# Performance work log

Hardware: AMD Instinct MI355X
Metric: run time of the kernel (lower is better)

Reference implementation:

```python
import jax, jax.numpy as jnp
import numpy as np

B, T, D = 2, 2048, 1024
H = 16
DH = D // H
SCALE = DH ** -0.5


def setup_inputs() -> dict:
    key = jax.random.key(0)
    ks = jax.random.split(key, 9)
    s = D ** -0.5
    return {
        "x": jax.random.normal(ks[0], (B, T, D), dtype=jnp.float32),
        "Wq": jax.random.normal(ks[1], (D, D), dtype=jnp.float32) * s,
        "bq": jax.random.normal(ks[2], (D,), dtype=jnp.float32) * 0.01,
        "Wk": jax.random.normal(ks[3], (D, D), dtype=jnp.float32) * s,
        "bk": jax.random.normal(ks[4], (D,), dtype=jnp.float32) * 0.01,
        "Wv": jax.random.normal(ks[5], (D, D), dtype=jnp.float32) * s,
        "bv": jax.random.normal(ks[6], (D,), dtype=jnp.float32) * 0.01,
        "Wo": jax.random.normal(ks[7], (D, D), dtype=jnp.float32) * s,
        "bo": jax.random.normal(ks[8], (D,), dtype=jnp.float32) * 0.01,
    }


def reference(x, Wq, bq, Wk, bk, Wv, bv, Wo, bo):
    # projections; torch Linear: y = x @ W.T + b. Here W is stored as (in, out).
    q = (x @ Wq + bq).reshape(B, T, H, DH).transpose(0, 2, 1, 3)  # (B,H,T,DH)
    k = (x @ Wk + bk).reshape(B, T, H, DH).transpose(0, 2, 1, 3)
    v = (x @ Wv + bv).reshape(B, T, H, DH).transpose(0, 2, 1, 3)
    scores = jnp.einsum("bhqd,bhkd->bhqk", q, k) * SCALE  # (B,H,T,T)
    causal = jnp.tril(jnp.ones((T, T), dtype=bool))
    scores = jnp.where(causal, scores, -jnp.inf)
    probs = jax.nn.softmax(scores, axis=-1)
    out = jnp.einsum("bhqk,bhkd->bhqd", probs, v)  # (B,H,T,DH)
    out = out.transpose(0, 2, 1, 3).reshape(B, T, D)
    out = out @ Wo + bo
    return out, (k, v)
```

## Files before the change

kernel.cpp:

```cpp
#include <hip/hip_runtime.h>

typedef float  f32x4  __attribute__((ext_vector_type(4)));
typedef float  f32x16 __attribute__((ext_vector_type(16)));
typedef __bf16 bf16x8 __attribute__((ext_vector_type(8)));
typedef short  s16x8  __attribute__((ext_vector_type(8)));
typedef short  s16x4  __attribute__((ext_vector_type(4)));
typedef unsigned int u32x4 __attribute__((ext_vector_type(4)));

static __device__ __forceinline__ unsigned short f2bf(float f) {
  return __builtin_bit_cast(unsigned short, (__bf16)f);
}
static __device__ __forceinline__ bf16x8 bc8(s16x8 v) {
  return __builtin_bit_cast(bf16x8, v);
}
static __device__ __forceinline__ f32x16 mfma32(bf16x8 a, bf16x8 b, f32x16 c) {
  return __builtin_amdgcn_mfma_f32_32x32x16_bf16(a, b, c, 0, 0, 0);
}
static __device__ __forceinline__ f32x4 mfma16(bf16x8 a, bf16x8 b, f32x4 c) {
  return __builtin_amdgcn_mfma_f32_16x16x32_bf16(a, b, c, 0, 0, 0);
}

static __device__ __forceinline__ void gl2lds16(const unsigned short* g, unsigned short* l) {
  __builtin_amdgcn_global_load_lds(
      (const __attribute__((address_space(1))) unsigned int*)g,
      (__attribute__((address_space(3))) unsigned int*)l, 16, 0, 0);
}

#define GSYNC(NSTR)                                          \
  do {                                                       \
    __builtin_amdgcn_sched_barrier(0);                       \
    asm volatile("s_waitcnt vmcnt(" NSTR ")" ::: "memory");  \
    __builtin_amdgcn_s_barrier();                            \
    __builtin_amdgcn_sched_barrier(0);                       \
  } while (0)

__global__ void prep_k(const float* __restrict__ x, unsigned short* __restrict__ xb,
                       const float* __restrict__ W0, const float* __restrict__ W1,
                       const float* __restrict__ W2, const float* __restrict__ W3,
                       unsigned short* __restrict__ wtb) {
  __shared__ unsigned short tl[64][72];
  const int bid = blockIdx.x;
  const int t = threadIdx.x;
  if (bid < 2048) {
    int i = (bid * 256 + t) * 8;
    float4 a = *(const float4*)(x + i);
    float4 b = *(const float4*)(x + i + 4);
    s16x8 o;
    o[0] = (short)f2bf(a.x); o[1] = (short)f2bf(a.y);
    o[2] = (short)f2bf(a.z); o[3] = (short)f2bf(a.w);
    o[4] = (short)f2bf(b.x); o[5] = (short)f2bf(b.y);
    o[6] = (short)f2bf(b.z); o[7] = (short)f2bf(b.w);
    *(s16x8*)(xb + i) = o;
    return;
  }
  const int rid = bid - 2048;
  const int z = rid >> 8, rem = rid & 255;
  const float* W = z == 0 ? W0 : z == 1 ? W1 : z == 2 ? W2 : W3;
  unsigned short* out = wtb + (size_t)z * 1048576;
  const int nt = (rem & 15) * 64, kt = (rem >> 4) * 64;
  const int row = t >> 2, seg = t & 3;
  const float* src = W + (kt + row) * 1024 + nt + seg * 16;
#pragma unroll
  for (int q = 0; q < 4; ++q) {
    float4 v = *(const float4*)(src + q * 4);
    tl[seg * 16 + q * 4 + 0][row] = f2bf(v.x);
    tl[seg * 16 + q * 4 + 1][row] = f2bf(v.y);
    tl[seg * 16 + q * 4 + 2][row] = f2bf(v.z);
    tl[seg * 16 + q * 4 + 3][row] = f2bf(v.w);
  }
  __syncthreads();
  unsigned short* dst = out + (nt + row) * 1024 + kt + seg * 16;
  *(s16x8*)dst       = *(const s16x8*)&tl[row][seg * 16];
  *(s16x8*)(dst + 8) = *(const s16x8*)&tl[row][seg * 16 + 8];
}

static __device__ __forceinline__ int trans_ix(int m, int n) {
  int b = m >> 11, tt = m & 2047, h = n >> 6, dh = n & 63;
  return ((b << 4) + h) * 131072 + tt * 64 + dh;
}

__global__ __launch_bounds__(512, 4) void gemm_qkv_k(const unsigned short* __restrict__ A,
                                                     const unsigned short* __restrict__ BT,
                                                     const float* __restrict__ b0,
                                                     const float* __restrict__ b1,
                                                     const float* __restrict__ b2,
                                                     float* __restrict__ outF,
                                                     unsigned short* __restrict__ oq,
                                                     unsigned short* __restrict__ ok,
                                                     unsigned short* __restrict__ ovT) {
  extern __shared__ unsigned short lds[];
  const int t = threadIdx.x;
  const int lane = t & 63, ln = lane & 15, g = lane >> 4;
  const int w = t >> 6, wm = w >> 2, wn = w & 3;
  const unsigned wgid = blockIdx.x;
  const unsigned swz = (wgid & 7) * 64 + (wgid >> 3);
  const int by = swz & 31, bx = swz >> 5;
  const int bm0 = by * 128, bn0 = bx * 192;

  const int ar = t >> 2;
  const unsigned short* aBase = A + (size_t)(bm0 + ar) * 1024 + (((t & 3) ^ ((ar >> 1) & 3)) * 8);
  const int br = t >> 3;
  const int bcol = (t & 7) ^ (br & 7);
  const unsigned short* bBase = BT + (size_t)(bn0 + br) * 1024 + bcol * 8;

  auto issueA = [&](int buf, int H, int kt) {
    gl2lds16(aBase + kt + H * 32, &lds[buf * 20480 + H * 4096 + t * 8]);
  };
  auto issueB = [&](int buf, int j, int kt) {
    gl2lds16(bBase + (size_t)j * 65536 + kt, &lds[buf * 20480 + 8192 + j * 4096 + t * 8]);
  };
  auto ldA = [&](int buf, int H, int mf) -> bf16x8 {
    const int row = wm * 64 + mf * 16 + ln;
    const int sp = g ^ ((row >> 1) & 3);
    return bc8(*(const s16x8*)&lds[buf * 20480 + H * 4096 + row * 32 + sp * 8]);
  };
  auto ldB = [&](int buf, int H, int nf) -> bf16x8 {
    const int row = wn * 48 + nf * 16 + ln;
    const int sp = (H * 4 + g) ^ (row & 7);
    return bc8(*(const s16x8*)&lds[buf * 20480 + 8192 + row * 64 + sp * 8]);
  };

  f32x4 acc[4][3] = {};
  issueA(0, 0, 0);
  issueB(0, 0, 0);
  issueB(0, 1, 0);
  issueB(0, 2, 0);
  issueA(0, 1, 0);

  for (int ti = 0; ti < 16; ++ti) {
    const int buf = ti & 1, nb = buf ^ 1;
    const bool hn = ti < 15;
    const int kn = (ti + 1) * 64;

    GSYNC("1");
    if (hn) { issueA(nb, 0, kn); issueB(nb, 0, kn); issueB(nb, 1, kn); }
    {
      bf16x8 afr[4], bfr[3];
#pragma unroll
      for (int mf = 0; mf < 4; ++mf) afr[mf] = ldA(buf, 0, mf);
#pragma unroll
      for (int nf = 0; nf < 3; ++nf) bfr[nf] = ldB(buf, 0, nf);
      __builtin_amdgcn_s_setprio(1);
#pragma unroll
      for (int mf = 0; mf < 4; ++mf)
#pragma unroll
        for (int nf = 0; nf < 3; ++nf) acc[mf][nf] = mfma16(afr[mf], bfr[nf], acc[mf][nf]);
      __builtin_amdgcn_s_setprio(0);
    }
    if (hn) GSYNC("3"); else GSYNC("0");
    if (hn) { issueB(nb, 2, kn); issueA(nb, 1, kn); }
    {
      bf16x8 afr[4], bfr[3];
#pragma unroll
      for (int mf = 0; mf < 4; ++mf) afr[mf] = ldA(buf, 1, mf);
#pragma unroll
      for (int nf = 0; nf < 3; ++nf) bfr[nf] = ldB(buf, 1, nf);
      __builtin_amdgcn_s_setprio(1);
#pragma unroll
      for (int mf = 0; mf < 4; ++mf)
#pragma unroll
        for (int nf = 0; nf < 3; ++nf) acc[mf][nf] = mfma16(afr[mf], bfr[nf], acc[mf][nf]);
      __builtin_amdgcn_s_setprio(0);
    }
  }

#pragma unroll
  for (int nf = 0; nf < 3; ++nf) {
    const int n = bn0 + wn * 48 + nf * 16 + ln;
    const int n1 = n & 1023;
    const float* bp = n < 1024 ? b0 : (n < 2048 ? b1 : b2);
    const float bias = bp[n1];
    if (n < 1024) {
#pragma unroll
      for (int mf = 0; mf < 4; ++mf)
#pragma unroll
        for (int r = 0; r < 4; ++r) {
          const int m = bm0 + wm * 64 + mf * 16 + g * 4 + r;
          oq[trans_ix(m, n1)] = f2bf((acc[mf][nf][r] + bias) * 0.18033688f);
        }
    } else if (n < 2048) {
#pragma unroll
      for (int mf = 0; mf < 4; ++mf)
#pragma unroll
        for (int r = 0; r < 4; ++r) {
          const int m = bm0 + wm * 64 + mf * 16 + g * 4 + r;
          const float v = acc[mf][nf][r] + bias;
          const int ix = trans_ix(m, n1);
          ok[ix] = f2bf(v);
          outF[4194304 + ix] = v;
        }
    } else {
      const int dh = n1 & 63, hh = n1 >> 6;
#pragma unroll
      for (int mf = 0; mf < 4; ++mf) {
        const int m0 = bm0 + wm * 64 + mf * 16 + g * 4;
        const int bb = m0 >> 11, tt = m0 & 2047;
        s16x4 pv;
#pragma unroll
        for (int r = 0; r < 4; ++r) {
          const float v = acc[mf][nf][r] + bias;
          outF[8388608 + trans_ix(m0 + r, n1)] = v;
          pv[r] = (short)f2bf(v);
        }
        *(s16x4*)(ovT + (size_t)((bb << 4) + hh) * 131072 + (size_t)dh * 2048 + tt) = pv;
      }
    }
  }
}

__global__ __launch_bounds__(512, 4) void gemm_o_k(const unsigned short* __restrict__ A,
                                                   const unsigned short* __restrict__ BT,
                                                   const float* __restrict__ b0,
                                                   float* __restrict__ outF) {
  extern __shared__ unsigned short lds[];
  const int t = threadIdx.x;
  const int lane = t & 63, ln = lane & 15, g = lane >> 4;
  const int w = t >> 6, wm = w >> 2, wn = w & 3;
  const unsigned wgid = blockIdx.x;
  const unsigned swz = (wgid & 7) * 64 + (wgid >> 3);
  const int bx = swz & 7, by = swz >> 3;
  const int bm0 = by * 64, bn0 = bx * 128;

  const int row = t >> 3;
  const int scol = (t & 7) ^ (row & 7);
  const unsigned short* aSrc = A + (size_t)(bm0 + row) * 1024 + scol * 8;
  const unsigned short* bSrc0 = BT + (size_t)(bn0 + row) * 1024 + scol * 8;
  const unsigned short* bSrc1 = BT + (size_t)(bn0 + 64 + row) * 1024 + scol * 8;

  auto issue3 = [&](int buf, int ti) {
    const int kt = ti * 64;
    gl2lds16(aSrc + kt, &lds[buf * 12288 + t * 8]);
    gl2lds16(bSrc0 + kt, &lds[buf * 12288 + 4096 + t * 8]);
    gl2lds16(bSrc1 + kt, &lds[buf * 12288 + 8192 + t * 8]);
  };
  auto ldA = [&](int buf, int H, int mf) -> bf16x8 {
    const int r = wm * 32 + mf * 16 + ln;
    const int sp = (H * 4 + g) ^ (r & 7);
    return bc8(*(const s16x8*)&lds[buf * 12288 + r * 64 + sp * 8]);
  };
  auto ldB = [&](int buf, int H, int nf) -> bf16x8 {
    const int r = wn * 32 + nf * 16 + ln;
    const int j = r >> 6, rl = r & 63;
    const int sp = (H * 4 + g) ^ (rl & 7);
    return bc8(*(const s16x8*)&lds[buf * 12288 + 4096 + j * 4096 + rl * 64 + sp * 8]);
  };

  f32x4 acc[2][2] = {};
  issue3(0, 0);
  issue3(1, 1);

  for (int i = 0; i < 16; ++i) {
    const int buf = i & 1;
    if (i < 15) GSYNC("3"); else GSYNC("0");
    bf16x8 a0[2], a1[2], bq0[2], bq1[2];
#pragma unroll
    for (int mf = 0; mf < 2; ++mf) { a0[mf] = ldA(buf, 0, mf); a1[mf] = ldA(buf, 1, mf); }
#pragma unroll
    for (int nf = 0; nf < 2; ++nf) { bq0[nf] = ldB(buf, 0, nf); bq1[nf] = ldB(buf, 1, nf); }
    asm volatile("s_waitcnt lgkmcnt(0)" ::: "memory");
    __builtin_amdgcn_sched_barrier(0);
    __builtin_amdgcn_s_barrier();
    __builtin_amdgcn_sched_barrier(0);
    if (i + 2 < 16) issue3(buf, i + 2);
    __builtin_amdgcn_s_setprio(1);
#pragma unroll
    for (int mf = 0; mf < 2; ++mf)
#pragma unroll
      for (int nf = 0; nf < 2; ++nf) {
        acc[mf][nf] = mfma16(a0[mf], bq0[nf], acc[mf][nf]);
        acc[mf][nf] = mfma16(a1[mf], bq1[nf], acc[mf][nf]);
      }
    __builtin_amdgcn_s_setprio(0);
  }

#pragma unroll
  for (int nf = 0; nf < 2; ++nf) {
    const int n = bn0 + wn * 32 + nf * 16 + ln;
    const float bias = b0[n];
#pragma unroll
    for (int mf = 0; mf < 2; ++mf)
#pragma unroll
      for (int r = 0; r < 4; ++r) {
        const int m = bm0 + wm * 32 + mf * 16 + g * 4 + r;
        outF[(size_t)m * 1024 + n] = acc[mf][nf][r] + bias;
      }
  }
}

__global__ __launch_bounds__(512) void attn_k(const unsigned short* __restrict__ qb,
                                              const unsigned short* __restrict__ kb,
                                              const unsigned short* __restrict__ vbT,
                                              unsigned short* __restrict__ ob) {
  extern __shared__ s16x8 kvS[];
  const int t = threadIdx.x;
  const int lane = t & 63, l31 = lane & 31, h5 = lane >> 5;
  const int w = t >> 6, grp = w >> 2, qw = w & 3;
  const unsigned wg = blockIdx.x;
  const int x = wg & 7, r_ = wg >> 3;
  const int bh = x + 8 * (r_ >> 3);
  const int p = r_ & 7;
  const int b = bh >> 4, h = bh & 15;
  const unsigned short* Qp = qb + (size_t)bh * 131072;
  const unsigned short* Kp = kb + (size_t)bh * 131072;
  const unsigned short* Vp = vbT + (size_t)bh * 131072;

  const int e0 = qw * 64 + lane;
  const int kr0 = e0 >> 3;
  const int kcol = (e0 & 7) ^ (kr0 & 7);
  const unsigned short* kSrc = Kp + (size_t)kr0 * 64 + kcol * 8;
  const unsigned short* vSrc = Vp + (size_t)kr0 * 2048 + kcol * 8;
  s16x8* gB = &kvS[grp * 3072];

  s16x8 onesv;
#pragma unroll
  for (int z = 0; z < 8; ++z) onesv[z] = (short)0x3F80;
  const bf16x8 onesf = bc8(onesv);

  float* mg0 = (float*)&kvS[0];
  float* mg1 = mg0 + 4352;
  float* ml  = mg0 + 8704;
  const int slot = qw * 64 + lane;

  for (int half = 0; half < 2; ++half) {
    const int qblk = half == 0 ? p : 15 - p;
    const int q0 = qblk * 128;
    const int NT = qblk + 1;
    const int tbase = grp * NT;
    const int qg = q0 + qw * 32 + l31;

    __syncthreads();

    bf16x8 qf[4];
#pragma unroll
    for (int m = 0; m < 4; ++m)
      qf[m] = bc8(*(const s16x8*)(Qp + (size_t)qg * 64 + 16 * m + 8 * h5));

    auto issue = [&](int ti, int buf) {
      const int kv0 = (tbase + ti) * 64;
      unsigned short* kd = (unsigned short*)&gB[buf * 1024];
      unsigned short* vd = (unsigned short*)&gB[buf * 1024 + 512];
      const unsigned short* ks = kSrc + (size_t)kv0 * 64;
      const unsigned short* vs = vSrc + kv0;
      gl2lds16(ks,         kd + e0 * 8);
      gl2lds16(ks + 2048,  kd + (e0 + 256) * 8);
      gl2lds16(vs,         vd + e0 * 8);
      gl2lds16(vs + 65536, vd + (e0 + 256) * 8);
    };

    issue(0, 0);
    if (NT > 1) issue(1, 1);

    f32x16 o0 = {}, o1 = {}, lsum = {};
    int buf = 0;
    for (int i = 0; i < NT; ++i) {
      if (i + 1 < NT) GSYNC("4"); else GSYNC("0");
      if (i + 2 < NT) issue(i + 2, buf == 0 ? 2 : buf - 1);
      const int kv0 = (tbase + i) * 64;
      const bool active = (kv0 <= q0 + qw * 32 + 31);
      if (active) {
        const s16x8* kb_ = &gB[buf * 1024];
        const s16x8* vb2 = &gB[buf * 1024 + 512];
        f32x16 s0 = {}, s1 = {};
#pragma unroll
        for (int m = 0; m < 4; ++m) {
          const int sl = 2 * m + h5;
          bf16x8 a0 = bc8(kb_[l31 * 8 + (sl ^ (l31 & 7))]);
          bf16x8 a1 = bc8(kb_[(l31 + 32) * 8 + (sl ^ (l31 & 7))]);
          s0 = mfma32(a0, qf[m], s0);
          s1 = mfma32(a1, qf[m], s1);
        }
        if (kv0 + 63 > q0 + qw * 32) {
#pragma unroll
          for (int r = 0; r < 16; ++r) {
            const int kvr = kv0 + (r & 3) + 8 * (r >> 2) + 4 * h5;
            if (kvr > qg) s0[r] = -1e30f;
            if (kvr + 32 > qg) s1[r] = -1e30f;
          }
        }
#pragma unroll
        for (int r = 0; r < 16; ++r) {
          s0[r] = __builtin_amdgcn_exp2f(s0[r]);
          s1[r] = __builtin_amdgcn_exp2f(s1[r]);
        }
        unsigned og[2][4][2];
#pragma unroll
        for (int gg = 0; gg < 4; ++gg) {
          asm("v_cvt_pk_bf16_f32 %0, %1, %2" : "=v"(og[0][gg][0]) : "v"(s0[4 * gg]),     "v"(s0[4 * gg + 1]));
          asm("v_cvt_pk_bf16_f32 %0, %1, %2" : "=v"(og[0][gg][1]) : "v"(s0[4 * gg + 2]), "v"(s0[4 * gg + 3]));
          asm("v_cvt_pk_bf16_f32 %0, %1, %2" : "=v"(og[1][gg][0]) : "v"(s1[4 * gg]),     "v"(s1[4 * gg + 1]));
          asm("v_cvt_pk_bf16_f32 %0, %1, %2" : "=v"(og[1][gg][1]) : "v"(s1[4 * gg + 2]), "v"(s1[4 * gg + 3]));
        }
        bf16x8 pf[4];
#pragma unroll
        for (int mp = 0; mp < 4; ++mp) {
          const int tau = mp >> 1, lc = mp & 1;
          unsigned a0 = og[tau][2 * lc][0], bq0 = og[tau][2 * lc + 1][0];
          unsigned a1 = og[tau][2 * lc][1], bq1 = og[tau][2 * lc + 1][1];
          asm volatile("v_permlane32_swap_b32 %0, %1" : "+v"(a0), "+v"(bq0));
          asm volatile("v_permlane32_swap_b32 %0, %1" : "+v"(a1), "+v"(bq1));
          u32x4 fw; fw[0] = a0; fw[1] = a1; fw[2] = bq0; fw[3] = bq1;
          pf[mp] = __builtin_bit_cast(bf16x8, fw);
        }
#pragma unroll
        for (int mp = 0; mp < 4; ++mp) {
          const int sl = 2 * mp + h5;
          bf16x8 va0 = bc8(vb2[l31 * 8 + (sl ^ (l31 & 7))]);
          bf16x8 va1 = bc8(vb2[(l31 + 32) * 8 + (sl ^ (l31 & 7))]);
          o0 = mfma32(va0, pf[mp], o0);
          o1 = mfma32(va1, pf[mp], o1);
          lsum = mfma32(onesf, pf[mp], lsum);
        }
      }
      buf = (buf == 2) ? 0 : buf + 1;
    }

    __syncthreads();
    if (grp == 1) {
#pragma unroll
      for (int r = 0; r < 16; ++r) mg0[slot * 17 + r] = o0[r];
#pragma unroll
      for (int r = 0; r < 16; ++r) mg1[slot * 17 + r] = o1[r];
      ml[slot] = lsum[0];
    }
    __syncthreads();
    if (grp == 0) {
      const float inv = 1.0f / (lsum[0] + ml[slot]);
      unsigned short* orow = ob + (size_t)(b * 2048 + qg) * 1024 + h * 64;
#pragma unroll
      for (int rq = 0; rq < 4; ++rq) {
        s16x4 ov0, ov1;
#pragma unroll
        for (int e = 0; e < 4; ++e) {
          ov0[e] = (short)f2bf((o0[4 * rq + e] + mg0[slot * 17 + 4 * rq + e]) * inv);
          ov1[e] = (short)f2bf((o1[4 * rq + e] + mg1[slot * 17 + 4 * rq + e]) * inv);
        }
        *(s16x4*)(orow + 8 * rq + 4 * h5)      = ov0;
        *(s16x4*)(orow + 32 + 8 * rq + 4 * h5) = ov1;
      }
    }
  }
}

extern "C" void kernel_launch(void* const* d_in, const int* in_sizes, int n_in,
                              void* d_out, int out_size, void* d_ws, size_t ws_size,
                              hipStream_t stream) {
  (void)in_sizes; (void)n_in; (void)out_size; (void)ws_size;
  const float* x  = (const float*)d_in[0];
  const float* Wq = (const float*)d_in[1];
  const float* bq = (const float*)d_in[2];
  const float* Wk = (const float*)d_in[3];
  const float* bk = (const float*)d_in[4];
  const float* Wv = (const float*)d_in[5];
  const float* bv = (const float*)d_in[6];
  const float* Wo = (const float*)d_in[7];
  const float* bo = (const float*)d_in[8];
  float* out = (float*)d_out;

  unsigned short* ws  = (unsigned short*)d_ws;
  unsigned short* xb  = ws;
  unsigned short* wtb = ws + 4194304;
  unsigned short* qbuf = ws + 8388608;
  unsigned short* kbuf = qbuf + 4194304;
  unsigned short* vbuf = kbuf + 4194304;
  unsigned short* ab   = vbuf + 4194304;

  prep_k<<<3072, 256, 0, stream>>>(x, xb, Wq, Wk, Wv, Wo, wtb);
  gemm_qkv_k<<<512, 512, 81920, stream>>>(xb, wtb, bq, bk, bv, out, qbuf, kbuf, vbuf);
  attn_k<<<256, 512, 98304, stream>>>(qbuf, kbuf, vbuf, ab);
  gemm_o_k<<<512, 512, 49152, stream>>>(ab, wtb + 3145728, bo, out);
}
```

Before: 95.74 us.

## Split attention KV loop across four wave groups with 1024-thread blocks

The attention kernel now launches 1024 threads per block, so four KV-splitting groups replace two. Each group takes every fourth 64-row KV tile, double-buffered in LDS behind a block-wide barrier per step, and the partial outputs are merged through shared memory at the end. It also raises wave priority around the MFMA sections. The aim is more parallelism within each block to cover load latency and the short causal rows, at the cost of a block-wide barrier every iteration, a larger LDS footprint (128 KB) and a heavier reduction.

```diff
diff --git a/kernel.cpp b/kernel.cpp
--- a/kernel.cpp
+++ b/kernel.cpp
@@ -287,10 +287,10 @@
   }
 }
 
-__global__ __launch_bounds__(512) void attn_k(const unsigned short* __restrict__ qb,
-                                              const unsigned short* __restrict__ kb,
-                                              const unsigned short* __restrict__ vbT,
-                                              unsigned short* __restrict__ ob) {
+__global__ __launch_bounds__(1024) void attn_k(const unsigned short* __restrict__ qb,
+                                               const unsigned short* __restrict__ kb,
+                                               const unsigned short* __restrict__ vbT,
+                                               unsigned short* __restrict__ ob) {
   extern __shared__ s16x8 kvS[];
   const int t = threadIdx.x;
   const int lane = t & 63, l31 = lane & 31, h5 = lane >> 5;
@@ -304,28 +304,26 @@
   const unsigned short* Kp = kb + (size_t)bh * 131072;
   const unsigned short* Vp = vbT + (size_t)bh * 131072;
 
-  const int e0 = qw * 64 + lane;
+  const int e0 = t & 255;
   const int kr0 = e0 >> 3;
   const int kcol = (e0 & 7) ^ (kr0 & 7);
   const unsigned short* kSrc = Kp + (size_t)kr0 * 64 + kcol * 8;
   const unsigned short* vSrc = Vp + (size_t)kr0 * 2048 + kcol * 8;
-  s16x8* gB = &kvS[grp * 3072];
+  s16x8* gB = &kvS[grp * 2048];
 
   s16x8 onesv;
 #pragma unroll
   for (int z = 0; z < 8; ++z) onesv[z] = (short)0x3F80;
   const bf16x8 onesf = bc8(onesv);
 
-  float* mg0 = (float*)&kvS[0];
-  float* mg1 = mg0 + 4352;
-  float* ml  = mg0 + 8704;
+  float* sc = (float*)kvS;
   const int slot = qw * 64 + lane;
 
   for (int half = 0; half < 2; ++half) {
     const int qblk = half == 0 ? p : 15 - p;
     const int q0 = qblk * 128;
-    const int NT = qblk + 1;
-    const int tbase = grp * NT;
+    const int N64 = 2 * qblk + 2;
+    const int NP = (N64 + 3) >> 2;
     const int qg = q0 + qw * 32 + l31;
 
     __syncthreads();
@@ -335,8 +333,8 @@
     for (int m = 0; m < 4; ++m)
       qf[m] = bc8(*(const s16x8*)(Qp + (size_t)qg * 64 + 16 * m + 8 * h5));
 
-    auto issue = [&](int ti, int buf) {
-      const int kv0 = (tbase + ti) * 64;
+    auto issue = [&](int T, int buf) {
+      const int kv0 = T * 64;
       unsigned short* kd = (unsigned short*)&gB[buf * 1024];
       unsigned short* vd = (unsigned short*)&gB[buf * 1024 + 512];
       const unsigned short* ks = kSrc + (size_t)kv0 * 64;
@@ -347,20 +345,28 @@
       gl2lds16(vs + 65536, vd + (e0 + 256) * 8);
     };
 
-    issue(0, 0);
-    if (NT > 1) issue(1, 1);
+    if (grp < N64) issue(grp, 0);
 
     f32x16 o0 = {}, o1 = {}, lsum = {};
-    int buf = 0;
-    for (int i = 0; i < NT; ++i) {
-      if (i + 1 < NT) GSYNC("4"); else GSYNC("0");
-      if (i + 2 < NT) issue(i + 2, buf == 0 ? 2 : buf - 1);
-      const int kv0 = (tbase + i) * 64;
-      const bool active = (kv0 <= q0 + qw * 32 + 31);
+
+    for (int i = 0; i < NP; ++i) {
+      __builtin_amdgcn_sched_barrier(0);
+      asm volatile("s_waitcnt vmcnt(0)" ::: "memory");
+      __builtin_amdgcn_s_barrier();
+      __builtin_amdgcn_sched_barrier(0);
+      {
+        const int Tn = 4 * (i + 1) + grp;
+        if (i + 1 < NP && Tn < N64) issue(Tn, (i + 1) & 1);
+      }
+      const int T = 4 * i + grp;
+      const int kv0 = T * 64;
+      const bool active = (T < N64) && (kv0 <= q0 + qw * 32 + 31);
       if (active) {
+        const int buf = i & 1;
         const s16x8* kb_ = &gB[buf * 1024];
         const s16x8* vb2 = &gB[buf * 1024 + 512];
         f32x16 s0 = {}, s1 = {};
+        __builtin_amdgcn_s_setprio(1);
 #pragma unroll
         for (int m = 0; m < 4; ++m) {
           const int sl = 2 * m + h5;
@@ -369,6 +375,7 @@
           s0 = mfma32(a0, qf[m], s0);
           s1 = mfma32(a1, qf[m], s1);
         }
+        __builtin_amdgcn_s_setprio(0);
         if (kv0 + 63 > q0 + qw * 32) {
 #pragma unroll
           for (int r = 0; r < 16; ++r) {
@@ -401,6 +408,7 @@
           u32x4 fw; fw[0] = a0; fw[1] = a1; fw[2] = bq0; fw[3] = bq1;
           pf[mp] = __builtin_bit_cast(bf16x8, fw);
         }
+        __builtin_amdgcn_s_setprio(1);
 #pragma unroll
         for (int mp = 0; mp < 4; ++mp) {
           const int sl = 2 * mp + h5;
@@ -410,29 +418,35 @@
           o1 = mfma32(va1, pf[mp], o1);
           lsum = mfma32(onesf, pf[mp], lsum);
         }
-      }
-      buf = (buf == 2) ? 0 : buf + 1;
+        __builtin_amdgcn_s_setprio(0);
+      }
     }
 
     __syncthreads();
-    if (grp == 1) {
-#pragma unroll
-      for (int r = 0; r < 16; ++r) mg0[slot * 17 + r] = o0[r];
-#pragma unroll
-      for (int r = 0; r < 16; ++r) mg1[slot * 17 + r] = o1[r];
-      ml[slot] = lsum[0];
+    if (grp > 0) {
+      float* dst = sc + (size_t)(grp - 1) * 8704 + (size_t)slot * 34;
+#pragma unroll
+      for (int r = 0; r < 8; ++r) {
+        *(float2*)(dst + 2 * r)      = make_float2(o0[2 * r], o0[2 * r + 1]);
+        *(float2*)(dst + 16 + 2 * r) = make_float2(o1[2 * r], o1[2 * r + 1]);
+      }
+      dst[32] = lsum[0];
     }
     __syncthreads();
     if (grp == 0) {
-      const float inv = 1.0f / (lsum[0] + ml[slot]);
+      const float* p0 = sc + (size_t)slot * 34;
+      const float* p1 = p0 + 8704;
+      const float* p2 = p1 + 8704;
+      const float inv = 1.0f / (lsum[0] + p0[32] + p1[32] + p2[32]);
       unsigned short* orow = ob + (size_t)(b * 2048 + qg) * 1024 + h * 64;
 #pragma unroll
       for (int rq = 0; rq < 4; ++rq) {
         s16x4 ov0, ov1;
 #pragma unroll
         for (int e = 0; e < 4; ++e) {
-          ov0[e] = (short)f2bf((o0[4 * rq + e] + mg0[slot * 17 + 4 * rq + e]) * inv);
-          ov1[e] = (short)f2bf((o1[4 * rq + e] + mg1[slot * 17 + 4 * rq + e]) * inv);
+          const int ei = 4 * rq + e;
+          ov0[e] = (short)f2bf((o0[ei] + p0[ei] + p1[ei] + p2[ei]) * inv);
+          ov1[e] = (short)f2bf((o1[ei] + p0[16 + ei] + p1[16 + ei] + p2[16 + ei]) * inv);
         }
         *(s16x4*)(orow + 8 * rq + 4 * h5)      = ov0;
         *(s16x4*)(orow + 32 + 8 * rq + 4 * h5) = ov1;
@@ -466,6 +480,6 @@
 
   prep_k<<<3072, 256, 0, stream>>>(x, xb, Wq, Wk, Wv, Wo, wtb);
   gemm_qkv_k<<<512, 512, 81920, stream>>>(xb, wtb, bq, bk, bv, out, qbuf, kbuf, vbuf);
-  attn_k<<<256, 512, 98304, stream>>>(qbuf, kbuf, vbuf, ab);
+  attn_k<<<256, 1024, 131072, stream>>>(qbuf, kbuf, vbuf, ab);
   gemm_o_k<<<512, 512, 49152, stream>>>(ab, wtb + 3145728, bo, out);
 }
```

Result: slower. 102.2 us (+6.8%).
